# Performance work log

Hardware: AMD Instinct MI355X
Metric: run time of the kernel (lower is better)

## Reference

```python
import jax, jax.numpy as jnp
import numpy as np

B, N, D = 2, 2048, 1024
H = 16
HD = D // H  # 64
NEG = -1e30


def setup_inputs() -> dict:
    key = jax.random.key(0)
    ks = jax.random.split(key, 6)
    s = 0.02
    return {
        "x": jax.random.normal(ks[0], (B, N, D), dtype=jnp.float32),
        "Wq": jax.random.normal(ks[1], (D, D), dtype=jnp.float32) * s,
        "Wk": jax.random.normal(ks[2], (D, D), dtype=jnp.float32) * s,
        "Wv": jax.random.normal(ks[3], (D, D), dtype=jnp.float32) * s,
        "Wo": jax.random.normal(ks[4], (D, D), dtype=jnp.float32) * s,
        "Wf": jax.random.normal(ks[5], (D, H), dtype=jnp.float32) * s,
    }


def reference(x, Wq, Wk, Wv, Wo, Wf):
    b, n, d = x.shape
    h, hd = H, HD
    scale = hd ** -0.5
    # projections (Linear without bias; weights stored as [in, out])
    q = (x @ Wq).reshape(b, n, h, hd).transpose(0, 2, 1, 3)  # b h n hd
    k = (x @ Wk).reshape(b, n, h, hd).transpose(0, 2, 1, 3)
    v = (x @ Wv).reshape(b, n, h, hd).transpose(0, 2, 1, 3)
    # per-head log forget gate, cumulative sum over positions
    log_f = jax.nn.log_sigmoid(x @ Wf).transpose(0, 2, 1)  # b h n
    c = jnp.cumsum(log_f, axis=-1)  # b h n
    # scores with additive decay bias: bias[i,j] = c[i] - c[j] (j <= i)
    scores = jnp.einsum('bhid,bhjd->bhij', q, k) * scale
    scores = scores + c[..., :, None] - c[..., None, :]
    causal = jnp.tril(jnp.ones((n, n), dtype=bool))
    scores = jnp.where(causal, scores, NEG)
    attn = jax.nn.softmax(scores, axis=-1)
    out = jnp.einsum('bhij,bhjd->bhid', attn, v)  # b h n hd
    out = out.transpose(0, 2, 1, 3).reshape(b, n, d)
    return out @ Wo
```

## Files before the change

kernel.cpp:

```cpp
#include <hip/hip_runtime.h>
#include <hip/hip_bf16.h>
#include <stdint.h>

#define NN 2048
#define DD 1024
#define HH 16
#define HDD 64
#define QBLK 64
#define KVBLK 64

typedef unsigned short u16;
typedef __attribute__((ext_vector_type(8))) __bf16 bf16x8_t;
typedef __attribute__((ext_vector_type(4))) float f32x4_t;

static __device__ __forceinline__ u16 f2bf(float f) {
  union { float f; uint32_t u; } v; v.f = f;
  uint32_t r = v.u + 0x7FFFu + ((v.u >> 16) & 1u);
  return (u16)(r >> 16);
}

static __device__ __forceinline__ void async_copy16(const void* g, void* l) {
  __builtin_amdgcn_global_load_lds((const __attribute__((address_space(1))) void*)g,
                                   (__attribute__((address_space(3))) void*)l, 16, 0, 0);
}

__global__ void transpose_w_kernel(const float* __restrict__ W0, const float* __restrict__ W1,
                                   const float* __restrict__ W2, const float* __restrict__ W3,
                                   u16* __restrict__ Wt) {
  __shared__ float tile[64][65];
  const float* W = blockIdx.y == 0 ? W0 : blockIdx.y == 1 ? W1 : blockIdx.y == 2 ? W2 : W3;
  u16* out = Wt + (size_t)blockIdx.y * DD * DD;
  int bx = blockIdx.x & 15;
  int by = blockIdx.x >> 4;
  int t = threadIdx.x;
  int c = t & 63, r4 = t >> 6;
#pragma unroll
  for (int i = 0; i < 16; i++) {
    int row = i * 4 + r4;
    tile[row][c] = W[(by * 64 + row) * DD + bx * 64 + c];
  }
  __syncthreads();
#pragma unroll
  for (int i = 0; i < 16; i++) {
    int row = i * 4 + r4;
    out[(bx * 64 + row) * DD + by * 64 + c] = f2bf(tile[c][row]);
  }
}

__global__ void logf_kernel(const float* __restrict__ x, const float* __restrict__ Wf,
                            float* __restrict__ lf, u16* __restrict__ xb) {
  __shared__ float xs[DD];
  __shared__ float part[16][17];
  int row = blockIdx.x;
  int t = threadIdx.x;
  float4 v = *(const float4*)&x[(size_t)row * DD + t * 4];
  *(float4*)&xs[t * 4] = v;
  ushort4 o;
  o.x = f2bf(v.x); o.y = f2bf(v.y); o.z = f2bf(v.z); o.w = f2bf(v.w);
  *(ushort4*)&xb[(size_t)row * DD + t * 4] = o;
  __syncthreads();
  int h = t & 15, chunk = t >> 4;
  float s = 0.f;
#pragma unroll 8
  for (int e = 0; e < 64; e++)
    s += xs[chunk * 64 + e] * Wf[(chunk * 64 + e) * HH + h];
  part[chunk][h] = s;
  __syncthreads();
  if (t < 16) {
    float z = 0.f;
#pragma unroll
    for (int i = 0; i < 16; i++) z += part[i][t];
    float ls = fminf(z, 0.f) - log1pf(__expf(-fabsf(z)));
    int b = row >> 11, n = row & (NN - 1);
    lf[(b * HH + t) * NN + n] = ls;
  }
}

__global__ void cumsum_kernel(const float* __restrict__ lf, float* __restrict__ c) {
  int bh = blockIdx.x;
  int lane = threadIdx.x;
  const float* in = lf + bh * NN;
  float* out = c + bh * NN;
  float carry = 0.f;
  for (int t0 = 0; t0 < NN; t0 += 256) {
    float4 v = *(const float4*)&in[t0 + lane * 4];
    float s1 = v.x + v.y, s2 = s1 + v.z, s3 = s2 + v.w;
    float incl = s3;
#pragma unroll
    for (int off = 1; off < 64; off <<= 1) {
      float u = __shfl_up(incl, off, 64);
      if (lane >= off) incl += u;
    }
    float excl = incl - s3 + carry;
    float4 o;
    o.x = excl + v.x; o.y = excl + s1; o.z = excl + s2; o.w = excl + s3;
    *(float4*)&out[t0 + lane * 4] = o;
    carry = __shfl(incl, 63, 64) + carry;
  }
}

__global__ __launch_bounds__(256) void gemm_kernel(const u16* __restrict__ A,
                                                   const u16* __restrict__ Wt,
                                                   u16* __restrict__ oQ, u16* __restrict__ oK,
                                                   u16* __restrict__ oV, float* __restrict__ oF,
                                                   int mode) {
  __shared__ u16 Als[128 * 64];
  __shared__ u16 Bls[128 * 64];
  int m0 = blockIdx.y * 128, n0 = blockIdx.x * 128;
  int tid = threadIdx.x;
  int lane = tid & 63, w = tid >> 6;
  int wm = w >> 1, wn = w & 1;
  int lr = lane & 15, lg = lane >> 4;

  const u16* gA[4]; const u16* gB[4]; u16* lA[4]; u16* lB[4];
#pragma unroll
  for (int j = 0; j < 4; j++) {
    int s = tid + j * 256;
    int row = s >> 3, ch = s & 7;
    int scol = (ch ^ (row & 7)) * 8;
    gA[j] = &A [(size_t)(m0 + row) * DD + scol];
    gB[j] = &Wt[(size_t)(n0 + row) * DD + scol];
    lA[j] = &Als[s * 8];
    lB[j] = &Bls[s * 8];
  }

  f32x4_t acc[4][4];
#pragma unroll
  for (int i = 0; i < 4; i++)
#pragma unroll
    for (int j = 0; j < 4; j++) acc[i][j] = (f32x4_t){0.f, 0.f, 0.f, 0.f};

  for (int kt = 0; kt < DD; kt += 64) {
    __syncthreads();
#pragma unroll
    for (int j = 0; j < 4; j++) {
      async_copy16(gA[j] + kt, lA[j]);
      async_copy16(gB[j] + kt, lB[j]);
    }
    __syncthreads();
#pragma unroll
    for (int kk = 0; kk < 2; kk++) {
      bf16x8_t af[4], bfv[4];
#pragma unroll
      for (int mi = 0; mi < 4; mi++) {
        int row = wm * 64 + mi * 16 + lr;
        int boff = (row * 128 + kk * 64 + lg * 16) ^ ((row & 7) << 4);
        af[mi] = *(const bf16x8_t*)((const char*)Als + boff);
      }
#pragma unroll
      for (int ni = 0; ni < 4; ni++) {
        int row = wn * 64 + ni * 16 + lr;
        int boff = (row * 128 + kk * 64 + lg * 16) ^ ((row & 7) << 4);
        bfv[ni] = *(const bf16x8_t*)((const char*)Bls + boff);
      }
#pragma unroll
      for (int mi = 0; mi < 4; mi++)
#pragma unroll
        for (int ni = 0; ni < 4; ni++)
          acc[mi][ni] = __builtin_amdgcn_mfma_f32_16x16x32_bf16(af[mi], bfv[ni], acc[mi][ni], 0, 0, 0);
    }
  }

  if (mode == 1) {
#pragma unroll
    for (int mi = 0; mi < 4; mi++)
#pragma unroll
      for (int ni = 0; ni < 4; ni++) {
        int gcol = n0 + wn * 64 + ni * 16 + lr;
#pragma unroll
        for (int r = 0; r < 4; r++) {
          int grow = m0 + wm * 64 + mi * 16 + lg * 4 + r;
          oF[(size_t)grow * DD + gcol] = acc[mi][ni][r];
        }
      }
  } else {
    int which = n0 >> 10;
    u16* outp = which == 0 ? oQ : which == 1 ? oK : oV;
    int nl0 = n0 & 1023;
#pragma unroll
    for (int mi = 0; mi < 4; mi++)
#pragma unroll
      for (int ni = 0; ni < 4; ni++) {
        int gcol = nl0 + wn * 64 + ni * 16 + lr;
        int h = gcol >> 6, hd = gcol & 63;
#pragma unroll
        for (int r = 0; r < 4; r++) {
          int grow = m0 + wm * 64 + mi * 16 + lg * 4 + r;
          int b = grow >> 11, n = grow & (NN - 1);
          outp[((size_t)(b * HH + h) * NN + n) * HDD + hd] = f2bf(acc[mi][ni][r]);
        }
      }
  }
}

__global__ void transpose_v_kernel(const u16* __restrict__ Vtmp, u16* __restrict__ Vt) {
  __shared__ u16 tile[64][80];
  int bh = blockIdx.y;
  int n0 = blockIdx.x * 64;
  int t = threadIdx.x;
  const u16* src = Vtmp + (size_t)bh * NN * HDD;
  u16* dst = Vt + (size_t)bh * HDD * NN;
#pragma unroll
  for (int it = 0; it < 2; it++) {
    int cc = t + it * 256;
    int row = cc >> 3, p = cc & 7;
    *(uint4*)&tile[row][p * 8] = *(const uint4*)&src[(size_t)(n0 + row) * HDD + p * 8];
  }
  __syncthreads();
#pragma unroll
  for (int it = 0; it < 2; it++) {
    int cc = t + it * 256;
    int row = cc >> 3, p = cc & 7;
    union { u16 v[8]; uint4 q; } tmp;
#pragma unroll
    for (int e = 0; e < 8; e++) tmp.v[e] = tile[p * 8 + e][row];
    *(uint4*)&dst[(size_t)row * NN + n0 + p * 8] = tmp.q;
  }
}

__global__ __launch_bounds__(256) void attn_kernel(const u16* __restrict__ Q,
                                                   const u16* __restrict__ K,
                                                   const u16* __restrict__ Vt,
                                                   const float* __restrict__ cw,
                                                   u16* __restrict__ O) {
  __shared__ u16 Kls[2][KVBLK * 64];
  __shared__ u16 Vls[2][64 * KVBLK];
  __shared__ u16 Pls[4][16 * 64];
  int pidx = blockIdx.x, bh = blockIdx.y;
  int tid = threadIdx.x;
  int lane = tid & 63, w = tid >> 6;
  int lr = lane & 15, lg = lane >> 4;
  const u16* Qh = Q + (size_t)bh * NN * HDD;
  const u16* Kh = K + (size_t)bh * NN * HDD;
  const u16* Vh = Vt + (size_t)bh * HDD * NN;
  const float* ch = cw + bh * NN;
  int b = bh >> 4, h = bh & 15;

  int s0 = tid, s1 = tid + 256;
  int r0 = s0 >> 3, p0 = s0 & 7;
  int r1 = s1 >> 3, p1 = s1 & 7;
  const u16* gk0 = &Kh[(size_t)r0 * HDD + ((p0 ^ (r0 & 7)) * 8)];
  const u16* gk1 = &Kh[(size_t)r1 * HDD + ((p1 ^ (r1 & 7)) * 8)];
  const u16* gv0 = &Vh[(size_t)r0 * NN + ((p0 ^ (r0 & 7)) * 8)];
  const u16* gv1 = &Vh[(size_t)r1 * NN + ((p1 ^ (r1 & 7)) * 8)];

  for (int which = 0; which < 2; which++) {
    int tile = which == 0 ? (31 - pidx) : pidx;
    int qb = tile * QBLK + w * 16;

    bf16x8_t qf[2];
#pragma unroll
    for (int s = 0; s < 2; s++)
      qf[s] = *(const bf16x8_t*)&Qh[(size_t)(qb + lr) * HDD + s * 32 + lg * 8];
    float cq[4];
#pragma unroll
    for (int r = 0; r < 4; r++) cq[r] = ch[qb + lg * 4 + r];

    float lsum[4] = {0.f, 0.f, 0.f, 0.f};
    f32x4_t oacc[4];
#pragma unroll
    for (int fn = 0; fn < 4; fn++) oacc[fn] = (f32x4_t){0.f, 0.f, 0.f, 0.f};

    async_copy16(gk0, &Kls[0][s0 * 8]);
    async_copy16(gk1, &Kls[0][s1 * 8]);
    async_copy16(gv0, &Vls[0][s0 * 8]);
    async_copy16(gv1, &Vls[0][s1 * 8]);
    __syncthreads();

    int cur = 0;
    for (int kvt = 0; kvt <= tile; kvt++) {
      if (kvt < tile) {
        int nb = cur ^ 1;
        size_t kvn = (size_t)(kvt + 1) * KVBLK;
        async_copy16(gk0 + kvn * HDD, &Kls[nb][s0 * 8]);
        async_copy16(gk1 + kvn * HDD, &Kls[nb][s1 * 8]);
        async_copy16(gv0 + kvn, &Vls[nb][s0 * 8]);
        async_copy16(gv1 + kvn, &Vls[nb][s1 * 8]);
      }
      int kv0 = kvt * KVBLK;
      const u16* Kb = Kls[cur];
      const u16* Vb = Vls[cur];
      float ck[4];
#pragma unroll
      for (int f = 0; f < 4; f++) ck[f] = ch[kv0 + f * 16 + lr];

      f32x4_t sacc[4];
#pragma unroll
      for (int f = 0; f < 4; f++) sacc[f] = (f32x4_t){0.f, 0.f, 0.f, 0.f};
#pragma unroll
      for (int f = 0; f < 4; f++) {
        int row = f * 16 + lr;
#pragma unroll
        for (int s = 0; s < 2; s++) {
          int boff = (row * 128 + s * 64 + lg * 16) ^ ((row & 7) << 4);
          bf16x8_t kf = *(const bf16x8_t*)((const char*)Kb + boff);
          sacc[f] = __builtin_amdgcn_mfma_f32_16x16x32_bf16(qf[s], kf, sacc[f], 0, 0, 0);
        }
      }

      bool diag = (kvt == tile);
      float pv[4][4];
#pragma unroll
      for (int f = 0; f < 4; f++) {
        int j = kv0 + f * 16 + lr;
#pragma unroll
        for (int r = 0; r < 4; r++) {
          float val = fmaf(sacc[f][r], 0.125f, cq[r] - ck[f]);
          float e = __expf(val);
          if (diag && j > qb + lg * 4 + r) e = 0.f;
          pv[f][r] = e; lsum[r] += e;
        }
      }

      u16* pw = (u16*)Pls[w];
#pragma unroll
      for (int f = 0; f < 4; f++)
#pragma unroll
        for (int r = 0; r < 4; r += 2) {
          __hip_bfloat162 h2 = __float22bfloat162_rn(make_float2(pv[f][r], pv[f][r + 1]));
          union { __hip_bfloat162 hh; uint32_t u; } cvt; cvt.hh = h2;
          int col = f * 16 + lr;
          int row0 = lg * 4 + r;
          int b0 = (row0 * 128 + col * 2) ^ ((row0 & 7) << 4);
          int row1 = row0 + 1;
          int b1 = (row1 * 128 + col * 2) ^ ((row1 & 7) << 4);
          *(u16*)((char*)pw + b0) = (u16)cvt.u;
          *(u16*)((char*)pw + b1) = (u16)(cvt.u >> 16);
        }
      bf16x8_t pa[2];
#pragma unroll
      for (int s = 0; s < 2; s++) {
        int boff = (lr * 128 + s * 64 + lg * 16) ^ ((lr & 7) << 4);
        pa[s] = *(const bf16x8_t*)((const char*)pw + boff);
      }
#pragma unroll
      for (int fn = 0; fn < 4; fn++) {
        int row = fn * 16 + lr;
#pragma unroll
        for (int s = 0; s < 2; s++) {
          int boff = (row * 128 + s * 64 + lg * 16) ^ ((row & 7) << 4);
          bf16x8_t vf = *(const bf16x8_t*)((const char*)Vb + boff);
          oacc[fn] = __builtin_amdgcn_mfma_f32_16x16x32_bf16(pa[s], vf, oacc[fn], 0, 0, 0);
        }
      }
      __syncthreads();
      cur ^= 1;
    }

#pragma unroll
    for (int mask = 1; mask < 16; mask <<= 1)
#pragma unroll
      for (int r = 0; r < 4; r++)
        lsum[r] += __shfl_xor(lsum[r], mask, 64);
    float rinv[4];
#pragma unroll
    for (int r = 0; r < 4; r++) rinv[r] = 1.0f / lsum[r];

#pragma unroll
    for (int fn = 0; fn < 4; fn++)
#pragma unroll
      for (int r = 0; r < 4; r++) {
        int n_idx = qb + lg * 4 + r;
        float v = oacc[fn][r] * rinv[r];
        O[((size_t)(b * NN + n_idx)) * DD + h * HDD + fn * 16 + lr] = f2bf(v);
      }
  }
}

extern "C" void kernel_launch(void* const* d_in, const int* in_sizes, int n_in,
                              void* d_out, int out_size, void* d_ws, size_t ws_size,
                              hipStream_t stream) {
  const float* x  = (const float*)d_in[0];
  const float* Wq = (const float*)d_in[1];
  const float* Wk = (const float*)d_in[2];
  const float* Wv = (const float*)d_in[3];
  const float* Wo = (const float*)d_in[4];
  const float* Wf = (const float*)d_in[5];
  float* out = (float*)d_out;
  char* ws = (char*)d_ws;
  const size_t MB = 1024 * 1024;
  u16* x_bf  = (u16*)(ws + 0);
  u16* WqkvT = (u16*)(ws + 8 * MB);
  u16* WoT   = (u16*)(ws + 14 * MB);
  u16* Qw    = (u16*)(ws + 16 * MB);
  u16* Kw    = (u16*)(ws + 24 * MB);
  u16* Vw    = (u16*)(ws + 32 * MB);
  u16* Ow    = (u16*)(ws + 40 * MB);
  float* lf  = (float*)(ws + 48 * MB);
  float* cwp = (float*)(ws + 48 * MB + 262144);
  u16* Vtmp  = (u16*)(ws + 49 * MB);

  transpose_w_kernel<<<dim3(256, 4), 256, 0, stream>>>(Wq, Wk, Wv, Wo, WqkvT);
  logf_kernel<<<4096, 256, 0, stream>>>(x, Wf, lf, x_bf);
  cumsum_kernel<<<32, 64, 0, stream>>>(lf, cwp);
  gemm_kernel<<<dim3(24, 32), 256, 0, stream>>>(x_bf, WqkvT, Qw, Kw, Vtmp, nullptr, 0);
  transpose_v_kernel<<<dim3(32, 32), 256, 0, stream>>>(Vtmp, Vw);
  attn_kernel<<<dim3(16, 32), 256, 0, stream>>>(Qw, Kw, Vw, cwp, Ow);
  gemm_kernel<<<dim3(8, 32), 256, 0, stream>>>(Ow, WqkvT + (size_t)3 * DD * DD, nullptr, nullptr, nullptr, out, 1);
}
```

Measured before the change: 141.2 us.

## Transpose attention MFMA operands, vectorize P/O stores, remap GEMM blocks, set MFMA priority

The attention kernel swaps the MFMA A/B operands so each lane owns one query row. This turns the row-sum into a two-step cross-lane reduction, lets the decay values load as float4, and lets the probabilities and output be written as packed vector stores instead of scattered 16-bit writes. The GEMM remaps workgroup indices in groups of eight for better cache locality, and both kernels raise wave priority around MFMA blocks. The aim is fewer LDS and global store instructions and shuffles, at the cost of more index arithmetic.

```diff
diff --git a/kernel.cpp b/kernel.cpp
--- a/kernel.cpp
+++ b/kernel.cpp
@@ -17,6 +17,12 @@
   union { float f; uint32_t u; } v; v.f = f;
   uint32_t r = v.u + 0x7FFFu + ((v.u >> 16) & 1u);
   return (u16)(r >> 16);
+}
+
+static __device__ __forceinline__ uint32_t packbf2(float a, float b) {
+  __hip_bfloat162 h2 = __float22bfloat162_rn(make_float2(a, b));
+  union { __hip_bfloat162 hh; uint32_t u; } cvt; cvt.hh = h2;
+  return cvt.u;
 }
 
 static __device__ __forceinline__ void async_copy16(const void* g, void* l) {
@@ -106,7 +112,11 @@
                                                    int mode) {
   __shared__ u16 Als[128 * 64];
   __shared__ u16 Bls[128 * 64];
-  int m0 = blockIdx.y * 128, n0 = blockIdx.x * 128;
+  int nwg = gridDim.x * gridDim.y;
+  int flat = blockIdx.y * gridDim.x + blockIdx.x;
+  int cpx = nwg >> 3;
+  int f2 = (flat & 7) * cpx + (flat >> 3);
+  int m0 = (f2 / gridDim.x) * 128, n0 = (f2 % gridDim.x) * 128;
   int tid = threadIdx.x;
   int lane = tid & 63, w = tid >> 6;
   int wm = w >> 1, wn = w & 1;
@@ -153,11 +163,13 @@
         int boff = (row * 128 + kk * 64 + lg * 16) ^ ((row & 7) << 4);
         bfv[ni] = *(const bf16x8_t*)((const char*)Bls + boff);
       }
+      __builtin_amdgcn_s_setprio(1);
 #pragma unroll
       for (int mi = 0; mi < 4; mi++)
 #pragma unroll
         for (int ni = 0; ni < 4; ni++)
           acc[mi][ni] = __builtin_amdgcn_mfma_f32_16x16x32_bf16(af[mi], bfv[ni], acc[mi][ni], 0, 0, 0);
+      __builtin_amdgcn_s_setprio(0);
     }
   }
 
@@ -247,16 +259,15 @@
   for (int which = 0; which < 2; which++) {
     int tile = which == 0 ? (31 - pidx) : pidx;
     int qb = tile * QBLK + w * 16;
+    int iq = qb + lr;
 
     bf16x8_t qf[2];
 #pragma unroll
     for (int s = 0; s < 2; s++)
-      qf[s] = *(const bf16x8_t*)&Qh[(size_t)(qb + lr) * HDD + s * 32 + lg * 8];
-    float cq[4];
-#pragma unroll
-    for (int r = 0; r < 4; r++) cq[r] = ch[qb + lg * 4 + r];
-
-    float lsum[4] = {0.f, 0.f, 0.f, 0.f};
+      qf[s] = *(const bf16x8_t*)&Qh[(size_t)iq * HDD + s * 32 + lg * 8];
+    float cq = ch[iq];
+
+    float lsum = 0.f;
     f32x4_t oacc[4];
 #pragma unroll
     for (int fn = 0; fn < 4; fn++) oacc[fn] = (f32x4_t){0.f, 0.f, 0.f, 0.f};
@@ -280,13 +291,15 @@
       int kv0 = kvt * KVBLK;
       const u16* Kb = Kls[cur];
       const u16* Vb = Vls[cur];
-      float ck[4];
-#pragma unroll
-      for (int f = 0; f < 4; f++) ck[f] = ch[kv0 + f * 16 + lr];
+      float4 ckv[4];
+#pragma unroll
+      for (int f = 0; f < 4; f++)
+        ckv[f] = *(const float4*)&ch[kv0 + f * 16 + lg * 4];
 
       f32x4_t sacc[4];
 #pragma unroll
       for (int f = 0; f < 4; f++) sacc[f] = (f32x4_t){0.f, 0.f, 0.f, 0.f};
+      __builtin_amdgcn_s_setprio(1);
 #pragma unroll
       for (int f = 0; f < 4; f++) {
         int row = f * 16 + lr;
@@ -294,45 +307,41 @@
         for (int s = 0; s < 2; s++) {
           int boff = (row * 128 + s * 64 + lg * 16) ^ ((row & 7) << 4);
           bf16x8_t kf = *(const bf16x8_t*)((const char*)Kb + boff);
-          sacc[f] = __builtin_amdgcn_mfma_f32_16x16x32_bf16(qf[s], kf, sacc[f], 0, 0, 0);
+          sacc[f] = __builtin_amdgcn_mfma_f32_16x16x32_bf16(kf, qf[s], sacc[f], 0, 0, 0);
         }
       }
+      __builtin_amdgcn_s_setprio(0);
 
       bool diag = (kvt == tile);
       float pv[4][4];
 #pragma unroll
       for (int f = 0; f < 4; f++) {
-        int j = kv0 + f * 16 + lr;
+        const float* ckp = &ckv[f].x;
 #pragma unroll
         for (int r = 0; r < 4; r++) {
-          float val = fmaf(sacc[f][r], 0.125f, cq[r] - ck[f]);
+          float val = fmaf(sacc[f][r], 0.125f, cq - ckp[r]);
           float e = __expf(val);
-          if (diag && j > qb + lg * 4 + r) e = 0.f;
-          pv[f][r] = e; lsum[r] += e;
+          if (diag && (kv0 + f * 16 + lg * 4 + r) > iq) e = 0.f;
+          pv[f][r] = e; lsum += e;
         }
       }
 
       u16* pw = (u16*)Pls[w];
 #pragma unroll
-      for (int f = 0; f < 4; f++)
-#pragma unroll
-        for (int r = 0; r < 4; r += 2) {
-          __hip_bfloat162 h2 = __float22bfloat162_rn(make_float2(pv[f][r], pv[f][r + 1]));
-          union { __hip_bfloat162 hh; uint32_t u; } cvt; cvt.hh = h2;
-          int col = f * 16 + lr;
-          int row0 = lg * 4 + r;
-          int b0 = (row0 * 128 + col * 2) ^ ((row0 & 7) << 4);
-          int row1 = row0 + 1;
-          int b1 = (row1 * 128 + col * 2) ^ ((row1 & 7) << 4);
-          *(u16*)((char*)pw + b0) = (u16)cvt.u;
-          *(u16*)((char*)pw + b1) = (u16)(cvt.u >> 16);
-        }
+      for (int f = 0; f < 4; f++) {
+        uint2 d2;
+        d2.x = packbf2(pv[f][0], pv[f][1]);
+        d2.y = packbf2(pv[f][2], pv[f][3]);
+        int boff = (lr * 128 + (f * 16 + lg * 4) * 2) ^ ((lr & 7) << 4);
+        *(uint2*)((char*)pw + boff) = d2;
+      }
       bf16x8_t pa[2];
 #pragma unroll
       for (int s = 0; s < 2; s++) {
         int boff = (lr * 128 + s * 64 + lg * 16) ^ ((lr & 7) << 4);
         pa[s] = *(const bf16x8_t*)((const char*)pw + boff);
       }
+      __builtin_amdgcn_s_setprio(1);
 #pragma unroll
       for (int fn = 0; fn < 4; fn++) {
         int row = fn * 16 + lr;
@@ -340,30 +349,28 @@
         for (int s = 0; s < 2; s++) {
           int boff = (row * 128 + s * 64 + lg * 16) ^ ((row & 7) << 4);
           bf16x8_t vf = *(const bf16x8_t*)((const char*)Vb + boff);
-          oacc[fn] = __builtin_amdgcn_mfma_f32_16x16x32_bf16(pa[s], vf, oacc[fn], 0, 0, 0);
+          oacc[fn] = __builtin_amdgcn_mfma_f32_16x16x32_bf16(vf, pa[s], oacc[fn], 0, 0, 0);
         }
       }
+      __builtin_amdgcn_s_setprio(0);
       __syncthreads();
       cur ^= 1;
     }
 
-#pragma unroll
-    for (int mask = 1; mask < 16; mask <<= 1)
-#pragma unroll
-      for (int r = 0; r < 4; r++)
-        lsum[r] += __shfl_xor(lsum[r], mask, 64);
-    float rinv[4];
-#pragma unroll
-    for (int r = 0; r < 4; r++) rinv[r] = 1.0f / lsum[r];
-
-#pragma unroll
-    for (int fn = 0; fn < 4; fn++)
-#pragma unroll
-      for (int r = 0; r < 4; r++) {
-        int n_idx = qb + lg * 4 + r;
-        float v = oacc[fn][r] * rinv[r];
-        O[((size_t)(b * NN + n_idx)) * DD + h * HDD + fn * 16 + lr] = f2bf(v);
-      }
+    lsum += __shfl_xor(lsum, 16, 64);
+    lsum += __shfl_xor(lsum, 32, 64);
+    float rinv = 1.0f / lsum;
+
+    u16* orow = O + ((size_t)(b * NN + iq)) * DD + h * HDD;
+#pragma unroll
+    for (int fn = 0; fn < 4; fn++) {
+      ushort4 o4;
+      o4.x = f2bf(oacc[fn][0] * rinv);
+      o4.y = f2bf(oacc[fn][1] * rinv);
+      o4.z = f2bf(oacc[fn][2] * rinv);
+      o4.w = f2bf(oacc[fn][3] * rinv);
+      *(ushort4*)&orow[fn * 16 + lg * 4] = o4;
+    }
   }
 }
 
```

New measurement: 147.6 us. +4.5%, slower.
